# Optimization experiments

Hardware: AMD Instinct MI355X
Metric: run time of the kernel (lower is better)

Reference implementation:

```python
import jax, jax.numpy as jnp
import numpy as np

HEADS = 8  # from init_kwargs; head_dim = dim // heads is only used as the softmax scale


def setup_inputs() -> dict:
    key = jax.random.key(0)
    k1, k2, k3, k4 = jax.random.split(key, 4)
    B, S, D = 16, 512, 256
    r1, r2 = 3, 16  # TT ranks: rank = [1, 3, 16, 1]
    x = jax.random.normal(k1, (B, S, D), jnp.float32)
    # TT factors of the stacked (3, D, D) QKV weight: (1,3,r1), (r1,D,r2), (r2,D,1)
    ar = jax.random.normal(k2, (1, 3, r1), jnp.float32) * 0.2
    br = jax.random.normal(k3, (r1, D, r2), jnp.float32) * 0.2
    cr = jax.random.normal(k4, (r2, D, 1), jnp.float32) * 0.2
    return {"x": x, "ar": ar, "br": br, "cr": cr}


def reference(x, ar, br, cr):
    B, S, D = x.shape
    r1 = ar.shape[2]           # == 3 (required by the final reshape in the torch code)
    r2 = cr.shape[0]
    Bp = B // r2               # grouped batch after split_heads
    head_dim = D // HEADS

    # df = stack([x,x,x]) -> (3,B,S,D), then view as (3, Bp, r2, S, D)
    x_r = x.reshape(Bp, r2, S, D)
    df5 = jnp.broadcast_to(x_r, (3, Bp, r2, S, D))  # no copy under XLA

    # matmul(df.permute(3,1,2,4,0), ar): contract the stack axis (k) with ar[0]
    t1 = jnp.einsum('kbqsd,ki->sbqdi', df5, ar[0])          # (S, Bp, r2, D, r1)

    # matmul(t1.permute(0,1,4,3,2), br.permute(0,2,1)): contract r2 (q) axis
    scores = jnp.einsum('sbqdi,ieq->sbide', t1, br)         # (S, Bp, r1, D, D)
    scores = scores / jnp.sqrt(jnp.float32(head_dim))
    attn = jax.nn.softmax(scores, axis=-1)                  # softmax over last D

    # matmul(attn, cr.permute(2,1,0)) then permute(2,1,4,0,3)
    out = jnp.einsum('sbide,qe->ibqsd', attn, cr[:, :, 0])  # (r1, Bp, r2, S, D)

    # reshape to (3, B, S, D) (valid since r1 == 3), sum over the stack axis
    out = out.reshape(3, B, S, D).sum(axis=0)               # (B, S, D)
    return out
```

## Files before the change

### kernel.cpp

```cpp
#include <hip/hip_runtime.h>
#include <hip/hip_bf16.h>
#include <math.h>


#define SS 512
#define DD 256
#define R2 16
#define NI 3

#define BR_UNITS (NI * 8 * 64)
#define CR_UNITS (16 * 64)
#define ALL_UNITS (BR_UNITS + CR_UNITS)
#define BR_USH (BR_UNITS * 8)
#define WS_USH (ALL_UNITS * 8)

typedef __attribute__((ext_vector_type(8))) short bf16x8;
typedef __attribute__((ext_vector_type(8))) unsigned short ushort8;
typedef __attribute__((ext_vector_type(16))) float f32x16;
typedef __attribute__((ext_vector_type(2))) unsigned uint2v;

union B8 { unsigned w[4]; bf16x8 v; };

static __device__ __forceinline__ unsigned short bf16bits(float f) {
    union { __hip_bfloat16 h; unsigned short u; } c;
    c.h = __float2bfloat16(f);
    return c.u;
}
static __device__ __forceinline__ unsigned packb(float a, float b) {
    union { __hip_bfloat162 h; unsigned u; } c;
    c.h = __float22bfloat162_rn(make_float2(a, b));
    return c.u;
}
static __device__ __forceinline__ unsigned permpack(float a, float b) {
    union { float f; unsigned u; } ua, ub;
    ua.f = a; ub.f = b;
    return __builtin_amdgcn_perm(ub.u, ua.u, 0x07060302u);
}

__global__ void tt_prep(const float* __restrict__ ar,
                        const float* __restrict__ br,
                        const float* __restrict__ cr,
                        unsigned short* __restrict__ wsf)
{
    const int t = blockIdx.x * 256 + threadIdx.x;
    float cA2[NI];
#pragma unroll
    for (int i = 0; i < NI; ++i) {
        float A = ar[0 * NI + i] + ar[1 * NI + i] + ar[2 * NI + i];
        cA2[i] = A * (0.17677669529663687f * 1.4426950408889634f);
    }
    if (t < BR_UNITS) {
        const int l = t & 63, et = (t >> 6) & 7, i = t >> 9;
        const float* src = br + (i * DD + et * 32 + (l & 31)) * R2 + 8 * (l >> 5);
        const float sc = cA2[i];
        ushort8 v;
#pragma unroll
        for (int j = 0; j < 8; ++j) v[j] = bf16bits(src[j] * sc);
        *(ushort8*)(wsf + t * 8) = v;
    } else {
        const int idx = t - BR_UNITS;
        const int l = idx & 63, h = (idx >> 6) & 1, et = idx >> 7;
        const int b = l & 31;
        ushort8 v;
#pragma unroll
        for (int j = 0; j < 8; ++j) {
            const int e = et * 32 + h * 16 + (j & 3) + 8 * (j >> 2) + 4 * (l >> 5);
            float val = (b < 16) ? cr[b * DD + e] : (b == 16 ? 1.0f : 0.0f);
            v[j] = bf16bits(val);
        }
        *(ushort8*)(wsf + (BR_USH + idx * 8)) = v;
    }
}

__global__ __launch_bounds__(256, 4) void tt_attn_mfma(
    const float* __restrict__ x,
    const unsigned short* __restrict__ wsf,
    float* __restrict__ out)
{
    __shared__ unsigned short lds[WS_USH];

    const int s     = blockIdx.x >> 1;
    const int dhalf = blockIdx.x & 1;
    const int tid   = threadIdx.x;
    const int lane  = tid & 63;
    const int wv    = tid >> 6;
    const int hi    = lane >> 5;
    const int d     = dhalf * 128 + wv * 32 + (lane & 31);

#pragma unroll
    for (int c = 0; c < 10; ++c) {
        const char* g = (const char*)wsf + (size_t)(c * 256 + tid) * 16;
        char* lp = (char*)lds + (size_t)(c * 256 + wv * 64) * 16;
        __builtin_amdgcn_global_load_lds(
            (const __attribute__((address_space(1))) void*)g,
            (__attribute__((address_space(3))) void*)lp, 16, 0, 0);
    }

    const float* xp = x + s * DD + d + (hi ? 8 * SS * DD : 0);
    float xr[8];
#pragma unroll
    for (int t = 0; t < 8; ++t) xr[t] = xp[t * SS * DD];
    B8 xb;
#pragma unroll
    for (int t = 0; t < 4; ++t) xb.w[t] = packb(xr[2 * t], xr[2 * t + 1]);
    const bf16x8 xf = xb.v;

    __syncthreads();

    f32x16 acc0{}, acc1{}, acc2{};
    const f32x16 zf{};

    const unsigned short* brl = lds + lane * 8;
    const unsigned short* crl = lds + BR_USH + lane * 8;

#pragma unroll 2
    for (int et = 0; et < 8; ++et) {
        const bf16x8 crA0 = *(const bf16x8*)(crl + (et * 2 + 0) * 512);
        const bf16x8 crA1 = *(const bf16x8*)(crl + (et * 2 + 1) * 512);
#pragma unroll
        for (int i = 0; i < NI; ++i) {
            const bf16x8 brA = *(const bf16x8*)(brl + (i * 8 + et) * 512);
            f32x16 g = __builtin_amdgcn_mfma_f32_32x32x16_bf16(brA, xf, zf, 0, 0, 0);
            float p[16];
#pragma unroll
            for (int r = 0; r < 16; ++r) p[r] = __builtin_amdgcn_exp2f(g[r]);
            B8 P0, P1;
            P0.w[0] = permpack(p[0],  p[1]);
            P0.w[1] = permpack(p[2],  p[3]);
            P0.w[2] = permpack(p[4],  p[5]);
            P0.w[3] = permpack(p[6],  p[7]);
            P1.w[0] = permpack(p[8],  p[9]);
            P1.w[1] = permpack(p[10], p[11]);
            P1.w[2] = permpack(p[12], p[13]);
            P1.w[3] = permpack(p[14], p[15]);
            if (i == 0) {
                acc0 = __builtin_amdgcn_mfma_f32_32x32x16_bf16(crA0, P0.v, acc0, 0, 0, 0);
                acc0 = __builtin_amdgcn_mfma_f32_32x32x16_bf16(crA1, P1.v, acc0, 0, 0, 0);
            } else if (i == 1) {
                acc1 = __builtin_amdgcn_mfma_f32_32x32x16_bf16(crA0, P0.v, acc1, 0, 0, 0);
                acc1 = __builtin_amdgcn_mfma_f32_32x32x16_bf16(crA1, P1.v, acc1, 0, 0, 0);
            } else {
                acc2 = __builtin_amdgcn_mfma_f32_32x32x16_bf16(crA0, P0.v, acc2, 0, 0, 0);
                acc2 = __builtin_amdgcn_mfma_f32_32x32x16_bf16(crA1, P1.v, acc2, 0, 0, 0);
            }
        }
    }

    float inv[NI];
#pragma unroll
    for (int i = 0; i < NI; ++i) {
        union { float f; unsigned u; } c;
        c.f = (i == 0) ? acc0[8] : (i == 1) ? acc1[8] : acc2[8];
        const uint2v r = __builtin_amdgcn_permlane32_swap(c.u, c.u, false, false);
        union { unsigned u; float f; } c2; c2.u = r.x;
        inv[i] = 1.0f / c2.f;
    }

#pragma unroll
    for (int r = 0; r < 8; ++r) {
        const int b = (r & 3) + 8 * (r >> 2) + 4 * hi;
        const float o = acc0[r] * inv[0] + acc1[r] * inv[1] + acc2[r] * inv[2];
        out[(b * SS + s) * DD + d] = o;
    }
}

extern "C" void kernel_launch(void* const* d_in, const int* in_sizes, int n_in,
                              void* d_out, int out_size, void* d_ws, size_t ws_size,
                              hipStream_t stream) {
    const float* x  = (const float*)d_in[0];
    const float* ar = (const float*)d_in[1];
    const float* br = (const float*)d_in[2];
    const float* cr = (const float*)d_in[3];
    float* out = (float*)d_out;

    unsigned short* wsf = (unsigned short*)d_ws;

    hipLaunchKernelGGL(tt_prep, dim3(10), dim3(256), 0, stream, ar, br, cr, wsf);
    hipLaunchKernelGGL(tt_attn_mfma, dim3(SS * 2), dim3(256), 0, stream, x, wsf, out);
}
```

Measured before the change: 22.59 us.

## Process two sequence positions per 512-thread block to amortize LDS weight staging

Each block now has 512 threads covering the full D dimension and loops over two consecutive sequence positions. The shared weight tiles are staged into LDS once and reused for both positions, so the grid shrinks from 1024 blocks to 256. This cuts redundant global-to-LDS copies and per-block setup. In exchange, only 256 blocks run on a 256-CU device and the two positions are processed serially, which may reduce latency hiding and occupancy.

```diff
diff --git a/kernel.cpp b/kernel.cpp
--- a/kernel.cpp
+++ b/kernel.cpp
@@ -72,95 +72,105 @@
     }
 }
 
-__global__ __launch_bounds__(256, 4) void tt_attn_mfma(
+__global__ __launch_bounds__(512, 2) void tt_attn_mfma(
     const float* __restrict__ x,
     const unsigned short* __restrict__ wsf,
     float* __restrict__ out)
 {
     __shared__ unsigned short lds[WS_USH];
 
-    const int s     = blockIdx.x >> 1;
-    const int dhalf = blockIdx.x & 1;
-    const int tid   = threadIdx.x;
-    const int lane  = tid & 63;
-    const int wv    = tid >> 6;
-    const int hi    = lane >> 5;
-    const int d     = dhalf * 128 + wv * 32 + (lane & 31);
+    const int tid  = threadIdx.x;
+    const int lane = tid & 63;
+    const int wv   = tid >> 6;
+    const int hi   = lane >> 5;
+    const int d    = (wv >> 2) * 128 + (wv & 3) * 32 + (lane & 31);
+    const int s0   = blockIdx.x * 2;
 
 #pragma unroll
-    for (int c = 0; c < 10; ++c) {
-        const char* g = (const char*)wsf + (size_t)(c * 256 + tid) * 16;
-        char* lp = (char*)lds + (size_t)(c * 256 + wv * 64) * 16;
+    for (int c = 0; c < 5; ++c) {
+        const char* g = (const char*)wsf + (size_t)(c * 512 + tid) * 16;
+        char* lp = (char*)lds + (size_t)(c * 512 + wv * 64) * 16;
         __builtin_amdgcn_global_load_lds(
             (const __attribute__((address_space(1))) void*)g,
             (__attribute__((address_space(3))) void*)lp, 16, 0, 0);
     }
 
-    const float* xp = x + s * DD + d + (hi ? 8 * SS * DD : 0);
-    float xr[8];
+    const float* xp = x + s0 * DD + d + (hi ? 8 * SS * DD : 0);
+    float xr0[8], xr1[8];
 #pragma unroll
-    for (int t = 0; t < 8; ++t) xr[t] = xp[t * SS * DD];
-    B8 xb;
+    for (int t = 0; t < 8; ++t) { xr0[t] = xp[t * SS * DD]; xr1[t] = xp[t * SS * DD + DD]; }
+    B8 xb0, xb1;
 #pragma unroll
-    for (int t = 0; t < 4; ++t) xb.w[t] = packb(xr[2 * t], xr[2 * t + 1]);
-    const bf16x8 xf = xb.v;
+    for (int t = 0; t < 4; ++t) {
+        xb0.w[t] = packb(xr0[2 * t], xr0[2 * t + 1]);
+        xb1.w[t] = packb(xr1[2 * t], xr1[2 * t + 1]);
+    }
 
     __syncthreads();
 
-    f32x16 acc0{}, acc1{}, acc2{};
+    const unsigned short* brl = lds + lane * 8;
+    const unsigned short* crl = lds + BR_USH + lane * 8;
     const f32x16 zf{};
 
-    const unsigned short* brl = lds + lane * 8;
-    const unsigned short* crl = lds + BR_USH + lane * 8;
+#pragma unroll 1
+    for (int r = 0; r < 2; ++r) {
+        B8 xsel;
+#pragma unroll
+        for (int t = 0; t < 4; ++t) xsel.w[t] = r ? xb1.w[t] : xb0.w[t];
+        const bf16x8 xf = xsel.v;
+
+        f32x16 acc0{}, acc1{}, acc2{};
 
 #pragma unroll 2
-    for (int et = 0; et < 8; ++et) {
-        const bf16x8 crA0 = *(const bf16x8*)(crl + (et * 2 + 0) * 512);
-        const bf16x8 crA1 = *(const bf16x8*)(crl + (et * 2 + 1) * 512);
+        for (int et = 0; et < 8; ++et) {
+            const bf16x8 crA0 = *(const bf16x8*)(crl + (et * 2 + 0) * 512);
+            const bf16x8 crA1 = *(const bf16x8*)(crl + (et * 2 + 1) * 512);
+#pragma unroll
+            for (int i = 0; i < NI; ++i) {
+                const bf16x8 brA = *(const bf16x8*)(brl + (i * 8 + et) * 512);
+                f32x16 g = __builtin_amdgcn_mfma_f32_32x32x16_bf16(brA, xf, zf, 0, 0, 0);
+                float p[16];
+#pragma unroll
+                for (int rr = 0; rr < 16; ++rr) p[rr] = __builtin_amdgcn_exp2f(g[rr]);
+                B8 P0, P1;
+                P0.w[0] = permpack(p[0],  p[1]);
+                P0.w[1] = permpack(p[2],  p[3]);
+                P0.w[2] = permpack(p[4],  p[5]);
+                P0.w[3] = permpack(p[6],  p[7]);
+                P1.w[0] = permpack(p[8],  p[9]);
+                P1.w[1] = permpack(p[10], p[11]);
+                P1.w[2] = permpack(p[12], p[13]);
+                P1.w[3] = permpack(p[14], p[15]);
+                if (i == 0) {
+                    acc0 = __builtin_amdgcn_mfma_f32_32x32x16_bf16(crA0, P0.v, acc0, 0, 0, 0);
+                    acc0 = __builtin_amdgcn_mfma_f32_32x32x16_bf16(crA1, P1.v, acc0, 0, 0, 0);
+                } else if (i == 1) {
+                    acc1 = __builtin_amdgcn_mfma_f32_32x32x16_bf16(crA0, P0.v, acc1, 0, 0, 0);
+                    acc1 = __builtin_amdgcn_mfma_f32_32x32x16_bf16(crA1, P1.v, acc1, 0, 0, 0);
+                } else {
+                    acc2 = __builtin_amdgcn_mfma_f32_32x32x16_bf16(crA0, P0.v, acc2, 0, 0, 0);
+                    acc2 = __builtin_amdgcn_mfma_f32_32x32x16_bf16(crA1, P1.v, acc2, 0, 0, 0);
+                }
+            }
+        }
+
+        float inv[NI];
 #pragma unroll
         for (int i = 0; i < NI; ++i) {
-            const bf16x8 brA = *(const bf16x8*)(brl + (i * 8 + et) * 512);
-            f32x16 g = __builtin_amdgcn_mfma_f32_32x32x16_bf16(brA, xf, zf, 0, 0, 0);
-            float p[16];
+            union { float f; unsigned u; } c;
+            c.f = (i == 0) ? acc0[8] : (i == 1) ? acc1[8] : acc2[8];
+            const uint2v rr = __builtin_amdgcn_permlane32_swap(c.u, c.u, false, false);
+            union { unsigned u; float f; } c2; c2.u = rr.x;
+            inv[i] = 1.0f / c2.f;
+        }
+
+        const int s = s0 + r;
 #pragma unroll
-            for (int r = 0; r < 16; ++r) p[r] = __builtin_amdgcn_exp2f(g[r]);
-            B8 P0, P1;
-            P0.w[0] = permpack(p[0],  p[1]);
-            P0.w[1] = permpack(p[2],  p[3]);
-            P0.w[2] = permpack(p[4],  p[5]);
-            P0.w[3] = permpack(p[6],  p[7]);
-            P1.w[0] = permpack(p[8],  p[9]);
-            P1.w[1] = permpack(p[10], p[11]);
-            P1.w[2] = permpack(p[12], p[13]);
-            P1.w[3] = permpack(p[14], p[15]);
-            if (i == 0) {
-                acc0 = __builtin_amdgcn_mfma_f32_32x32x16_bf16(crA0, P0.v, acc0, 0, 0, 0);
-                acc0 = __builtin_amdgcn_mfma_f32_32x32x16_bf16(crA1, P1.v, acc0, 0, 0, 0);
-            } else if (i == 1) {
-                acc1 = __builtin_amdgcn_mfma_f32_32x32x16_bf16(crA0, P0.v, acc1, 0, 0, 0);
-                acc1 = __builtin_amdgcn_mfma_f32_32x32x16_bf16(crA1, P1.v, acc1, 0, 0, 0);
-            } else {
-                acc2 = __builtin_amdgcn_mfma_f32_32x32x16_bf16(crA0, P0.v, acc2, 0, 0, 0);
-                acc2 = __builtin_amdgcn_mfma_f32_32x32x16_bf16(crA1, P1.v, acc2, 0, 0, 0);
-            }
+        for (int rr = 0; rr < 8; ++rr) {
+            const int b = (rr & 3) + 8 * (rr >> 2) + 4 * hi;
+            const float o = acc0[rr] * inv[0] + acc1[rr] * inv[1] + acc2[rr] * inv[2];
+            out[(b * SS + s) * DD + d] = o;
         }
-    }
-
-    float inv[NI];
-#pragma unroll
-    for (int i = 0; i < NI; ++i) {
-        union { float f; unsigned u; } c;
-        c.f = (i == 0) ? acc0[8] : (i == 1) ? acc1[8] : acc2[8];
-        const uint2v r = __builtin_amdgcn_permlane32_swap(c.u, c.u, false, false);
-        union { unsigned u; float f; } c2; c2.u = r.x;
-        inv[i] = 1.0f / c2.f;
-    }
-
-#pragma unroll
-    for (int r = 0; r < 8; ++r) {
-        const int b = (r & 3) + 8 * (r >> 2) + 4 * hi;
-        const float o = acc0[r] * inv[0] + acc1[r] * inv[1] + acc2[r] * inv[2];
-        out[(b * SS + s) * DD + d] = o;
     }
 }
 
@@ -176,5 +186,5 @@
     unsigned short* wsf = (unsigned short*)d_ws;
 
     hipLaunchKernelGGL(tt_prep, dim3(10), dim3(256), 0, stream, ar, br, cr, wsf);
-    hipLaunchKernelGGL(tt_attn_mfma, dim3(SS * 2), dim3(256), 0, stream, x, wsf, out);
+    hipLaunchKernelGGL(tt_attn_mfma, dim3(SS / 2), dim3(512), 0, stream, x, wsf, out);
 }
```

Measured after the change: 23.25 us. 2.9% more time.

## Process two sequence positions per block to reuse LDS weight operands

Applied to the files above, without the earlier changes.

Each block now handles two consecutive s positions instead of one, which halves the grid to 512 blocks. The br/cr operands read from LDS feed twice as many MFMAs, and the per-block LDS fill of the prepared weights is amortized over twice the work. In exchange, register pressure roughly doubles (six accumulators), so launch bounds drop to 2 blocks per SM, and there are fewer blocks to hide latency.

```diff
diff --git a/kernel.cpp b/kernel.cpp
--- a/kernel.cpp
+++ b/kernel.cpp
@@ -72,15 +72,16 @@
     }
 }
 
-__global__ __launch_bounds__(256, 4) void tt_attn_mfma(
+__global__ __launch_bounds__(256, 2) void tt_attn_mfma(
     const float* __restrict__ x,
     const unsigned short* __restrict__ wsf,
     float* __restrict__ out)
 {
     __shared__ unsigned short lds[WS_USH];
 
-    const int s     = blockIdx.x >> 1;
+    const int sp    = blockIdx.x >> 1;
     const int dhalf = blockIdx.x & 1;
+    const int s0    = sp * 2;
     const int tid   = threadIdx.x;
     const int lane  = tid & 63;
     const int wv    = tid >> 6;
@@ -96,18 +97,25 @@
             (__attribute__((address_space(3))) void*)lp, 16, 0, 0);
     }
 
-    const float* xp = x + s * DD + d + (hi ? 8 * SS * DD : 0);
-    float xr[8];
-#pragma unroll
-    for (int t = 0; t < 8; ++t) xr[t] = xp[t * SS * DD];
-    B8 xb;
-#pragma unroll
-    for (int t = 0; t < 4; ++t) xb.w[t] = packb(xr[2 * t], xr[2 * t + 1]);
-    const bf16x8 xf = xb.v;
+    const float* xp = x + s0 * DD + d + (hi ? 8 * SS * DD : 0);
+    float xr0[8], xr1[8];
+#pragma unroll
+    for (int t = 0; t < 8; ++t) {
+        xr0[t] = xp[t * SS * DD];
+        xr1[t] = xp[t * SS * DD + DD];
+    }
+    B8 xb0, xb1;
+#pragma unroll
+    for (int t = 0; t < 4; ++t) {
+        xb0.w[t] = packb(xr0[2 * t], xr0[2 * t + 1]);
+        xb1.w[t] = packb(xr1[2 * t], xr1[2 * t + 1]);
+    }
+    const bf16x8 xf0 = xb0.v, xf1 = xb1.v;
 
     __syncthreads();
 
-    f32x16 acc0{}, acc1{}, acc2{};
+    f32x16 a00{}, a10{}, a20{};
+    f32x16 a01{}, a11{}, a21{};
     const f32x16 zf{};
 
     const unsigned short* brl = lds + lane * 8;
@@ -120,47 +128,62 @@
 #pragma unroll
         for (int i = 0; i < NI; ++i) {
             const bf16x8 brA = *(const bf16x8*)(brl + (i * 8 + et) * 512);
-            f32x16 g = __builtin_amdgcn_mfma_f32_32x32x16_bf16(brA, xf, zf, 0, 0, 0);
-            float p[16];
-#pragma unroll
-            for (int r = 0; r < 16; ++r) p[r] = __builtin_amdgcn_exp2f(g[r]);
-            B8 P0, P1;
-            P0.w[0] = permpack(p[0],  p[1]);
-            P0.w[1] = permpack(p[2],  p[3]);
-            P0.w[2] = permpack(p[4],  p[5]);
-            P0.w[3] = permpack(p[6],  p[7]);
-            P1.w[0] = permpack(p[8],  p[9]);
-            P1.w[1] = permpack(p[10], p[11]);
-            P1.w[2] = permpack(p[12], p[13]);
-            P1.w[3] = permpack(p[14], p[15]);
+            f32x16 g0 = __builtin_amdgcn_mfma_f32_32x32x16_bf16(brA, xf0, zf, 0, 0, 0);
+            f32x16 g1 = __builtin_amdgcn_mfma_f32_32x32x16_bf16(brA, xf1, zf, 0, 0, 0);
+            float p0[16], p1[16];
+#pragma unroll
+            for (int rr = 0; rr < 16; ++rr) {
+                p0[rr] = __builtin_amdgcn_exp2f(g0[rr]);
+                p1[rr] = __builtin_amdgcn_exp2f(g1[rr]);
+            }
+            B8 A0, B0, A1, B1;
+#pragma unroll
+            for (int rr = 0; rr < 4; ++rr) {
+                A0.w[rr] = permpack(p0[2 * rr],     p0[2 * rr + 1]);
+                B0.w[rr] = permpack(p0[2 * rr + 8], p0[2 * rr + 9]);
+                A1.w[rr] = permpack(p1[2 * rr],     p1[2 * rr + 1]);
+                B1.w[rr] = permpack(p1[2 * rr + 8], p1[2 * rr + 9]);
+            }
             if (i == 0) {
-                acc0 = __builtin_amdgcn_mfma_f32_32x32x16_bf16(crA0, P0.v, acc0, 0, 0, 0);
-                acc0 = __builtin_amdgcn_mfma_f32_32x32x16_bf16(crA1, P1.v, acc0, 0, 0, 0);
+                a00 = __builtin_amdgcn_mfma_f32_32x32x16_bf16(crA0, A0.v, a00, 0, 0, 0);
+                a00 = __builtin_amdgcn_mfma_f32_32x32x16_bf16(crA1, B0.v, a00, 0, 0, 0);
+                a01 = __builtin_amdgcn_mfma_f32_32x32x16_bf16(crA0, A1.v, a01, 0, 0, 0);
+                a01 = __builtin_amdgcn_mfma_f32_32x32x16_bf16(crA1, B1.v, a01, 0, 0, 0);
             } else if (i == 1) {
-                acc1 = __builtin_amdgcn_mfma_f32_32x32x16_bf16(crA0, P0.v, acc1, 0, 0, 0);
-                acc1 = __builtin_amdgcn_mfma_f32_32x32x16_bf16(crA1, P1.v, acc1, 0, 0, 0);
+                a10 = __builtin_amdgcn_mfma_f32_32x32x16_bf16(crA0, A0.v, a10, 0, 0, 0);
+                a10 = __builtin_amdgcn_mfma_f32_32x32x16_bf16(crA1, B0.v, a10, 0, 0, 0);
+                a11 = __builtin_amdgcn_mfma_f32_32x32x16_bf16(crA0, A1.v, a11, 0, 0, 0);
+                a11 = __builtin_amdgcn_mfma_f32_32x32x16_bf16(crA1, B1.v, a11, 0, 0, 0);
             } else {
-                acc2 = __builtin_amdgcn_mfma_f32_32x32x16_bf16(crA0, P0.v, acc2, 0, 0, 0);
-                acc2 = __builtin_amdgcn_mfma_f32_32x32x16_bf16(crA1, P1.v, acc2, 0, 0, 0);
+                a20 = __builtin_amdgcn_mfma_f32_32x32x16_bf16(crA0, A0.v, a20, 0, 0, 0);
+                a20 = __builtin_amdgcn_mfma_f32_32x32x16_bf16(crA1, B0.v, a20, 0, 0, 0);
+                a21 = __builtin_amdgcn_mfma_f32_32x32x16_bf16(crA0, A1.v, a21, 0, 0, 0);
+                a21 = __builtin_amdgcn_mfma_f32_32x32x16_bf16(crA1, B1.v, a21, 0, 0, 0);
             }
         }
     }
 
-    float inv[NI];
+    float inv0[NI], inv1[NI];
 #pragma unroll
     for (int i = 0; i < NI; ++i) {
-        union { float f; unsigned u; } c;
-        c.f = (i == 0) ? acc0[8] : (i == 1) ? acc1[8] : acc2[8];
-        const uint2v r = __builtin_amdgcn_permlane32_swap(c.u, c.u, false, false);
-        union { unsigned u; float f; } c2; c2.u = r.x;
-        inv[i] = 1.0f / c2.f;
-    }
-
-#pragma unroll
-    for (int r = 0; r < 8; ++r) {
-        const int b = (r & 3) + 8 * (r >> 2) + 4 * hi;
-        const float o = acc0[r] * inv[0] + acc1[r] * inv[1] + acc2[r] * inv[2];
-        out[(b * SS + s) * DD + d] = o;
+        union { float f; unsigned u; } c0, c1;
+        c0.f = (i == 0) ? a00[8] : (i == 1) ? a10[8] : a20[8];
+        c1.f = (i == 0) ? a01[8] : (i == 1) ? a11[8] : a21[8];
+        const uint2v r0 = __builtin_amdgcn_permlane32_swap(c0.u, c0.u, false, false);
+        const uint2v r1 = __builtin_amdgcn_permlane32_swap(c1.u, c1.u, false, false);
+        union { unsigned u; float f; } d0, d1;
+        d0.u = r0.x; d1.u = r1.x;
+        inv0[i] = 1.0f / d0.f;
+        inv1[i] = 1.0f / d1.f;
+    }
+
+#pragma unroll
+    for (int rr = 0; rr < 8; ++rr) {
+        const int b = (rr & 3) + 8 * (rr >> 2) + 4 * hi;
+        const float o0 = a00[rr] * inv0[0] + a10[rr] * inv0[1] + a20[rr] * inv0[2];
+        const float o1 = a01[rr] * inv1[0] + a11[rr] * inv1[1] + a21[rr] * inv1[2];
+        out[(b * SS + s0) * DD + d]     = o0;
+        out[(b * SS + s0 + 1) * DD + d] = o1;
     }
 }
 
@@ -176,5 +199,5 @@
     unsigned short* wsf = (unsigned short*)d_ws;
 
     hipLaunchKernelGGL(tt_prep, dim3(10), dim3(256), 0, stream, ar, br, cr, wsf);
-    hipLaunchKernelGGL(tt_attn_mfma, dim3(SS * 2), dim3(256), 0, stream, x, wsf, out);
-}
+    hipLaunchKernelGGL(tt_attn_mfma, dim3(SS), dim3(256), 0, stream, x, wsf, out);
+}
```

After: 23.20 us. +2.7%, slower.
